# Optimization experiments

Measured on AMD Instinct MI355X. Metric: run time of the kernel, lower is better.

Reference implementation:

```python
import jax, jax.numpy as jnp
import numpy as np

B, N, IN_DIM, OUT_DIM, H = 8, 1024, 256, 256, 8
D = OUT_DIM // H  # support_dim = 32


def setup_inputs() -> dict:
    key = jax.random.key(0)
    k_a, k_x, k_w, k_f1, k_f2 = jax.random.split(key, 5)
    A = (jax.random.uniform(k_a, (B, N, N)) < 0.05).astype(jnp.float32)
    eye = jnp.eye(N, dtype=jnp.float32)
    A = jnp.maximum(A, eye[None, :, :])
    X = jax.random.normal(k_x, (B, N, IN_DIM), dtype=jnp.float32)
    std_w = 1.0 / np.sqrt(OUT_DIM)
    std_f = 1.0 / np.sqrt(D)
    weight = jax.random.uniform(k_w, (IN_DIM, OUT_DIM), minval=-std_w, maxval=std_w)
    fc1 = jax.random.uniform(k_f1, (H, D), minval=-std_f, maxval=std_f)
    fc2 = jax.random.uniform(k_f2, (H, D), minval=-std_f, maxval=std_f)
    return {"A": A, "X": X, "weight": weight, "fc1": fc1, "fc2": fc2}


def reference(A, X, weight, fc1, fc2):
    # inputs: [B, N, H, D]
    inputs = jnp.einsum('bni,io->bno', X, weight).reshape(B, N, H, D)
    # additive attention scores (rank-1 broadcast)
    self_s = jnp.einsum('bnhd,hd->bhn', inputs, fc1)   # [B,H,N] (query/self term)
    neigh_s = jnp.einsum('bnhd,hd->bhn', inputs, fc2)  # [B,H,N] (key/neighbor term)
    scores = jax.nn.leaky_relu(self_s[:, :, :, None] + neigh_s[:, :, None, :])  # [B,H,N,N]
    mask = (-1e9 * (1.0 - A))[:, None, :, :]  # [B,1,N,N]
    alphas = jax.nn.softmax(scores + mask, axis=-1)  # [B,H,N,N]
    out = jnp.einsum('bhnm,bmhd->bnhd', alphas, inputs).reshape(B, N, OUT_DIM)
    return jax.nn.relu(out)
```

## Files before the change

### kernel.cpp

```cpp
#include <hip/hip_runtime.h>

typedef unsigned short u16;
typedef __attribute__((ext_vector_type(8))) short short8;
typedef __attribute__((ext_vector_type(4))) float floatx4;

#define NB 8
#define NN 1024
#define KDIM 256
#define ODIM 256
#define NH 8
#define LDA 264
#define ECAP 256
#define ESTR 260

__device__ __forceinline__ u16 bf_rne(float x) {
    union { float f; unsigned u; } c{x};
    unsigned r = c.u + 0x7fff + ((c.u >> 16) & 1);
    return (u16)(r >> 16);
}
__device__ __forceinline__ float bf_f(u16 b) {
    union { unsigned u; float f; } c{(unsigned)b << 16};
    return c.f;
}

__global__ __launch_bounds__(256) void wprep(const float* __restrict__ W,
                                             u16* __restrict__ WhiT,
                                             u16* __restrict__ WloT) {
    __shared__ float tile[64][65];
    int bt = blockIdx.x;
    int kt = bt >> 2, ot = bt & 3;
    int tid = threadIdx.x;
    int r = tid >> 6, c = tid & 63;
#pragma unroll
    for (int rr = r; rr < 64; rr += 4)
        tile[rr][c] = W[(kt * 64 + rr) * ODIM + ot * 64 + c];
    __syncthreads();
#pragma unroll
    for (int oo = r; oo < 64; oo += 4) {
        float w = tile[c][oo];
        u16 h = bf_rne(w);
        u16 l = bf_rne(w - bf_f(h));
        WhiT[(ot * 64 + oo) * KDIM + kt * 64 + c] = h;
        WloT[(ot * 64 + oo) * KDIM + kt * 64 + c] = l;
    }
}

__global__ __launch_bounds__(256) void gemm_scores(
        const float* __restrict__ X, const u16* __restrict__ WhiT,
        const u16* __restrict__ WloT, const float* __restrict__ fc1,
        const float* __restrict__ fc2, float* __restrict__ inp,
        float* __restrict__ self_s, float* __restrict__ neigh_s) {
    __shared__ u16 ah_lds[16 * LDA];
    __shared__ u16 al_lds[16 * LDA];

    int tid = threadIdx.x;
    int w = tid >> 6, lane = tid & 63;
    int m = lane & 15, q = lane >> 4;
    int row0 = blockIdx.x * 16;

    const float4* Xr = (const float4*)(X + (size_t)row0 * KDIM);
#pragma unroll
    for (int p = 0; p < 4; ++p) {
        int f = p * 256 + tid;
        int r = f >> 6, c4 = (f & 63) * 4;
        float4 v = Xr[f];
        ushort4 hi, lo; u16 hh, ll;
#define SPLIT1(val, A, B) hh = bf_rne(val); ll = bf_rne((val) - bf_f(hh)); A = hh; B = ll;
        SPLIT1(v.x, hi.x, lo.x)
        SPLIT1(v.y, hi.y, lo.y)
        SPLIT1(v.z, hi.z, lo.z)
        SPLIT1(v.w, hi.w, lo.w)
        *(ushort4*)&ah_lds[r * LDA + c4] = hi;
        *(ushort4*)&al_lds[r * LDA + c4] = lo;
    }
    __syncthreads();

    floatx4 acc[4] = {{0,0,0,0},{0,0,0,0},{0,0,0,0},{0,0,0,0}};
#pragma unroll
    for (int k0 = 0; k0 < KDIM; k0 += 32) {
        short8 Ah = *(const short8*)&ah_lds[m * LDA + k0 + q * 8];
        short8 Al = *(const short8*)&al_lds[m * LDA + k0 + q * 8];
#pragma unroll
        for (int t = 0; t < 4; ++t) {
            int o = w * 64 + t * 16 + m;
            short8 Bh = *(const short8*)(WhiT + (size_t)o * KDIM + k0 + q * 8);
            short8 Bl = *(const short8*)(WloT + (size_t)o * KDIM + k0 + q * 8);
            acc[t] = __builtin_amdgcn_mfma_f32_16x16x32_bf16(Ah, Bh, acc[t], 0, 0, 0);
            acc[t] = __builtin_amdgcn_mfma_f32_16x16x32_bf16(Ah, Bl, acc[t], 0, 0, 0);
            acc[t] = __builtin_amdgcn_mfma_f32_16x16x32_bf16(Al, Bh, acc[t], 0, 0, 0);
        }
    }

#pragma unroll
    for (int t = 0; t < 4; ++t) {
        int col = w * 64 + t * 16 + m;
#pragma unroll
        for (int r = 0; r < 4; ++r)
            inp[(size_t)(row0 + q * 4 + r) * ODIM + col] = acc[t][r];
    }

    float f1[4], f2[4];
#pragma unroll
    for (int t = 0; t < 4; ++t) {
        int col = w * 64 + t * 16 + m;
        f1[t] = fc1[col];
        f2[t] = fc2[col];
    }
#pragma unroll
    for (int r = 0; r < 4; ++r) {
        float a0 = acc[0][r] * f1[0] + acc[1][r] * f1[1];
        float b0 = acc[0][r] * f2[0] + acc[1][r] * f2[1];
        float a1 = acc[2][r] * f1[2] + acc[3][r] * f1[3];
        float b1 = acc[2][r] * f2[2] + acc[3][r] * f2[3];
#pragma unroll
        for (int ofs = 8; ofs >= 1; ofs >>= 1) {
            a0 += __shfl_xor(a0, ofs);
            b0 += __shfl_xor(b0, ofs);
            a1 += __shfl_xor(a1, ofs);
            b1 += __shfl_xor(b1, ofs);
        }
        if (m == 0) {
            int n = row0 + q * 4 + r;
            int b = n >> 10, nn = n & 1023;
            self_s [((size_t)(b * NH + 2 * w) << 10) + nn] = a0;
            neigh_s[((size_t)(b * NH + 2 * w) << 10) + nn] = b0;
            self_s [((size_t)(b * NH + 2 * w + 1) << 10) + nn] = a1;
            neigh_s[((size_t)(b * NH + 2 * w + 1) << 10) + nn] = b1;
        }
    }
}

__global__ __launch_bounds__(256) void gat_agg(
        const float* __restrict__ A, const float* __restrict__ inp,
        const float* __restrict__ self_s, const float* __restrict__ neigh_s,
        float* __restrict__ out) {
    __shared__ u16 lst[NN];
    __shared__ float esc[NH][ESTR];
    __shared__ float red[4][256];
    __shared__ float hinv[NH];
    __shared__ int cnt;

    int bx = blockIdx.x;
    int b = bx & 7;
    int n = bx >> 3;
    int bn = (b << 10) | n;
    int tid = threadIdx.x;

    if (tid == 0) cnt = 0;
    __syncthreads();
    {
        float4 a4 = ((const float4*)(A + (size_t)bn * NN))[tid];
        int base = tid * 4;
        if (a4.x != 0.f) lst[atomicAdd(&cnt, 1)] = (u16)base;
        if (a4.y != 0.f) lst[atomicAdd(&cnt, 1)] = (u16)(base + 1);
        if (a4.z != 0.f) lst[atomicAdd(&cnt, 1)] = (u16)(base + 2);
        if (a4.w != 0.f) lst[atomicAdd(&cnt, 1)] = (u16)(base + 3);
    }
    __syncthreads();
    int nnz = cnt;
    if (nnz > ECAP) nnz = ECAP;

    int h = tid >> 5, j = tid & 31;
    const float* nsh = neigh_s + ((size_t)(b * NH + h) << 10);
    float selfv = self_s[((size_t)(b * NH + h) << 10) + n];
    float lsum = 0.f;
    for (int i = j; i < nnz; i += 32) {
        float s = selfv + nsh[lst[i]];
        s = s > 0.f ? s : 0.01f * s;
        float e = __expf(s);
        esc[h][i] = e;
        lsum += e;
    }
#pragma unroll
    for (int ofs = 16; ofs >= 1; ofs >>= 1)
        lsum += __shfl_xor(lsum, ofs);
    if (j == 0) hinv[h] = 1.f / lsum;
    __syncthreads();

    int wv = tid >> 6, lane = tid & 63;
    int hh = lane >> 3;
    const float4* ib = (const float4*)(inp + ((size_t)b << 10) * ODIM) + lane;
    floatx4 acc = {0.f, 0.f, 0.f, 0.f};
#pragma unroll 2
    for (int i = wv; i < nnz; i += 4) {
        float e = esc[hh][i];
        float4 v = ib[(size_t)lst[i] * 64];
        acc[0] = fmaf(e, v.x, acc[0]);
        acc[1] = fmaf(e, v.y, acc[1]);
        acc[2] = fmaf(e, v.z, acc[2]);
        acc[3] = fmaf(e, v.w, acc[3]);
    }
    *(floatx4*)&red[wv][lane * 4] = acc;
    __syncthreads();

    float r0 = red[0][tid] + red[1][tid] + red[2][tid] + red[3][tid];
    r0 *= hinv[tid >> 5];
    out[(size_t)bn * ODIM + tid] = r0 > 0.f ? r0 : 0.f;
}

extern "C" void kernel_launch(void* const* d_in, const int* in_sizes, int n_in,
                              void* d_out, int out_size, void* d_ws, size_t ws_size,
                              hipStream_t stream) {
    const float* A   = (const float*)d_in[0];
    const float* X   = (const float*)d_in[1];
    const float* W   = (const float*)d_in[2];
    const float* fc1 = (const float*)d_in[3];
    const float* fc2 = (const float*)d_in[4];
    float* out = (float*)d_out;

    char* ws = (char*)d_ws;
    const size_t MB = 1024u * 1024u;
    float* inp     = (float*)ws;
    u16*   WhiT    = (u16*)(ws + 8 * MB);
    u16*   WloT    = (u16*)(ws + 8 * MB + 128 * 1024);
    float* self_s  = (float*)(ws + 8 * MB + 256 * 1024);
    float* neigh_s = (float*)(ws + 8 * MB + 512 * 1024);

    wprep<<<16, 256, 0, stream>>>(W, WhiT, WloT);
    gemm_scores<<<NB * NN / 16, 256, 0, stream>>>(
        X, WhiT, WloT, fc1, fc2, inp, self_s, neigh_s);
    gat_agg<<<NB * NN, 256, 0, stream>>>(A, inp, self_s, neigh_s, out);
}
```

Baseline: 131.7 us.

## Fuse weight prep, GEMM and aggregation into one cooperative persistent kernel

Replaces the three launches with a single cooperative kernel of 1024 blocks that uses grid-wide syncs between weight splitting, the split-bf16 GEMM with score reduction, and the attention aggregation. Each block now covers half the output columns of a 16-row tile in the GEMM, then processes 8 destination rows in a loop for aggregation. The aim is to remove launch gaps and inter-kernel tails. In exchange it adds grid-sync cost and runs the aggregation with fewer, persistent blocks, which may hide memory latency less well. The old three-kernel path is kept as a fallback if the cooperative launch fails.

```diff
diff --git a/kernel.cpp b/kernel.cpp
--- a/kernel.cpp
+++ b/kernel.cpp
@@ -1,4 +1,7 @@
 #include <hip/hip_runtime.h>
+#include <hip/hip_cooperative_groups.h>
+
+namespace cg = cooperative_groups;
 
 typedef unsigned short u16;
 typedef __attribute__((ext_vector_type(8))) short short8;
@@ -22,6 +25,182 @@
     union { unsigned u; float f; } c{(unsigned)b << 16};
     return c.f;
 }
+#define SPLIT1(val, A_, B_) { u16 hh_ = bf_rne(val); u16 ll_ = bf_rne((val) - bf_f(hh_)); A_ = hh_; B_ = ll_; }
+
+__global__ __launch_bounds__(256, 4) void gat_fused(
+        const float* __restrict__ A, const float* __restrict__ X,
+        const float* __restrict__ W, const float* __restrict__ fc1,
+        const float* __restrict__ fc2, float* __restrict__ inp,
+        u16* __restrict__ WhiT, u16* __restrict__ WloT,
+        float* __restrict__ self_s, float* __restrict__ neigh_s,
+        float* __restrict__ out) {
+    __shared__ __align__(16) char smem[17408];
+    u16* ah_lds = (u16*)smem;
+    u16* al_lds = ah_lds + 16 * LDA;
+
+    int tid = threadIdx.x;
+    int bid = blockIdx.x;
+    int w = tid >> 6, lane = tid & 63;
+    int m = lane & 15, q = lane >> 4;
+
+    cg::grid_group grid = cg::this_grid();
+
+    if (bid < 16) {
+        float (*wtile)[65] = (float(*)[65])smem;
+        int kt = bid >> 2, ot = bid & 3;
+        int r = tid >> 6, c = tid & 63;
+#pragma unroll
+        for (int rr = r; rr < 64; rr += 4)
+            wtile[rr][c] = W[(kt * 64 + rr) * ODIM + ot * 64 + c];
+        __syncthreads();
+#pragma unroll
+        for (int oo = r; oo < 64; oo += 4) {
+            float wv = wtile[c][oo];
+            u16 h, l;
+            SPLIT1(wv, h, l)
+            WhiT[(ot * 64 + oo) * KDIM + kt * 64 + c] = h;
+            WloT[(ot * 64 + oo) * KDIM + kt * 64 + c] = l;
+        }
+        __syncthreads();
+    }
+
+    int rb = bid >> 1;
+    int row0 = rb * 16;
+    int cbase = (bid & 1) * 128;
+    {
+        const float4* Xr = (const float4*)(X + (size_t)row0 * KDIM);
+#pragma unroll
+        for (int p = 0; p < 4; ++p) {
+            int f = p * 256 + tid;
+            int r = f >> 6, c4 = (f & 63) * 4;
+            float4 v = Xr[f];
+            ushort4 hi, lo;
+            SPLIT1(v.x, hi.x, lo.x)
+            SPLIT1(v.y, hi.y, lo.y)
+            SPLIT1(v.z, hi.z, lo.z)
+            SPLIT1(v.w, hi.w, lo.w)
+            *(ushort4*)&ah_lds[r * LDA + c4] = hi;
+            *(ushort4*)&al_lds[r * LDA + c4] = lo;
+        }
+    }
+    if (bid < 16) __threadfence();
+    grid.sync();
+
+    floatx4 acc[2] = {{0, 0, 0, 0}, {0, 0, 0, 0}};
+#pragma unroll
+    for (int k0 = 0; k0 < KDIM; k0 += 32) {
+        short8 Ah = *(const short8*)&ah_lds[m * LDA + k0 + q * 8];
+        short8 Al = *(const short8*)&al_lds[m * LDA + k0 + q * 8];
+#pragma unroll
+        for (int t = 0; t < 2; ++t) {
+            int o = cbase + w * 32 + t * 16 + m;
+            short8 Bh = *(const short8*)(WhiT + (size_t)o * KDIM + k0 + q * 8);
+            short8 Bl = *(const short8*)(WloT + (size_t)o * KDIM + k0 + q * 8);
+            acc[t] = __builtin_amdgcn_mfma_f32_16x16x32_bf16(Ah, Bh, acc[t], 0, 0, 0);
+            acc[t] = __builtin_amdgcn_mfma_f32_16x16x32_bf16(Ah, Bl, acc[t], 0, 0, 0);
+            acc[t] = __builtin_amdgcn_mfma_f32_16x16x32_bf16(Al, Bh, acc[t], 0, 0, 0);
+        }
+    }
+#pragma unroll
+    for (int t = 0; t < 2; ++t) {
+        int col = cbase + w * 32 + t * 16 + m;
+#pragma unroll
+        for (int r = 0; r < 4; ++r)
+            inp[(size_t)(row0 + q * 4 + r) * ODIM + col] = acc[t][r];
+    }
+    {
+        int hd = (bid & 1) * 4 + w;
+        float f1[2], f2[2];
+#pragma unroll
+        for (int t = 0; t < 2; ++t) {
+            int col = hd * 32 + t * 16 + m;
+            f1[t] = fc1[col];
+            f2[t] = fc2[col];
+        }
+#pragma unroll
+        for (int r = 0; r < 4; ++r) {
+            float a = acc[0][r] * f1[0] + acc[1][r] * f1[1];
+            float bb = acc[0][r] * f2[0] + acc[1][r] * f2[1];
+#pragma unroll
+            for (int ofs = 8; ofs >= 1; ofs >>= 1) {
+                a += __shfl_xor(a, ofs);
+                bb += __shfl_xor(bb, ofs);
+            }
+            if (m == 0) {
+                int n = row0 + q * 4 + r;
+                int b = n >> 10, nn = n & 1023;
+                self_s [((size_t)(b * NH + hd) << 10) + nn] = a;
+                neigh_s[((size_t)(b * NH + hd) << 10) + nn] = bb;
+            }
+        }
+    }
+    __threadfence();
+    grid.sync();
+
+    u16*  lst  = (u16*)smem;
+    float* esc = (float*)(smem + 2048);
+    float* red = (float*)(smem + 10368);
+    float* hinv = (float*)(smem + 14464);
+    int*  cntp = (int*)(smem + 14496);
+
+    int b2 = bid >> 7;
+    int h = tid >> 5, j = tid & 31;
+    int hh = lane >> 3;
+    const float4* ib = (const float4*)(inp + ((size_t)b2 << 10) * ODIM) + lane;
+
+    for (int rr = 0; rr < 8; ++rr) {
+        int bn = bid * 8 + rr;
+        int n = bn & 1023;
+
+        if (tid == 0) *cntp = 0;
+        __syncthreads();
+        {
+            float4 a4 = ((const float4*)(A + (size_t)bn * NN))[tid];
+            int base = tid * 4;
+            if (a4.x != 0.f) lst[atomicAdd(cntp, 1)] = (u16)base;
+            if (a4.y != 0.f) lst[atomicAdd(cntp, 1)] = (u16)(base + 1);
+            if (a4.z != 0.f) lst[atomicAdd(cntp, 1)] = (u16)(base + 2);
+            if (a4.w != 0.f) lst[atomicAdd(cntp, 1)] = (u16)(base + 3);
+        }
+        __syncthreads();
+        int nnz = *cntp;
+        if (nnz > ECAP) nnz = ECAP;
+
+        const float* nsh = neigh_s + ((size_t)(b2 * NH + h) << 10);
+        float selfv = self_s[((size_t)(b2 * NH + h) << 10) + n];
+        float lsum = 0.f;
+        for (int i = j; i < nnz; i += 32) {
+            float s = selfv + nsh[lst[i]];
+            s = s > 0.f ? s : 0.01f * s;
+            float e = __expf(s);
+            esc[h * ESTR + i] = e;
+            lsum += e;
+        }
+#pragma unroll
+        for (int ofs = 16; ofs >= 1; ofs >>= 1)
+            lsum += __shfl_xor(lsum, ofs);
+        if (j == 0) hinv[h] = 1.f / lsum;
+        __syncthreads();
+
+        floatx4 acc2 = {0.f, 0.f, 0.f, 0.f};
+#pragma unroll 4
+        for (int i = w; i < nnz; i += 4) {
+            float e = esc[hh * ESTR + i];
+            float4 v = ib[(size_t)lst[i] * 64];
+            acc2[0] = fmaf(e, v.x, acc2[0]);
+            acc2[1] = fmaf(e, v.y, acc2[1]);
+            acc2[2] = fmaf(e, v.z, acc2[2]);
+            acc2[3] = fmaf(e, v.w, acc2[3]);
+        }
+        *(floatx4*)&red[w * 256 + lane * 4] = acc2;
+        __syncthreads();
+
+        float r0 = red[tid] + red[256 + tid] + red[512 + tid] + red[768 + tid];
+        r0 *= hinv[tid >> 5];
+        out[(size_t)bn * ODIM + tid] = r0 > 0.f ? r0 : 0.f;
+        __syncthreads();
+    }
+}
 
 __global__ __launch_bounds__(256) void wprep(const float* __restrict__ W,
                                              u16* __restrict__ WhiT,
@@ -38,8 +217,8 @@
 #pragma unroll
     for (int oo = r; oo < 64; oo += 4) {
         float w = tile[c][oo];
-        u16 h = bf_rne(w);
-        u16 l = bf_rne(w - bf_f(h));
+        u16 h, l;
+        SPLIT1(w, h, l)
         WhiT[(ot * 64 + oo) * KDIM + kt * 64 + c] = h;
         WloT[(ot * 64 + oo) * KDIM + kt * 64 + c] = l;
     }
@@ -64,8 +243,7 @@
         int f = p * 256 + tid;
         int r = f >> 6, c4 = (f & 63) * 4;
         float4 v = Xr[f];
-        ushort4 hi, lo; u16 hh, ll;
-#define SPLIT1(val, A, B) hh = bf_rne(val); ll = bf_rne((val) - bf_f(hh)); A = hh; B = ll;
+        ushort4 hi, lo;
         SPLIT1(v.x, hi.x, lo.x)
         SPLIT1(v.y, hi.y, lo.y)
         SPLIT1(v.z, hi.z, lo.z)
@@ -216,8 +394,16 @@
     float* self_s  = (float*)(ws + 8 * MB + 256 * 1024);
     float* neigh_s = (float*)(ws + 8 * MB + 512 * 1024);
 
-    wprep<<<16, 256, 0, stream>>>(W, WhiT, WloT);
-    gemm_scores<<<NB * NN / 16, 256, 0, stream>>>(
-        X, WhiT, WloT, fc1, fc2, inp, self_s, neigh_s);
-    gat_agg<<<NB * NN, 256, 0, stream>>>(A, inp, self_s, neigh_s, out);
-}
+    void* args[] = {(void*)&A, (void*)&X, (void*)&W, (void*)&fc1, (void*)&fc2,
+                    (void*)&inp, (void*)&WhiT, (void*)&WloT, (void*)&self_s,
+                    (void*)&neigh_s, (void*)&out};
+    hipError_t e = hipLaunchCooperativeKernel((const void*)gat_fused,
+                                              dim3(1024), dim3(256),
+                                              args, 0, stream);
+    if (e != hipSuccess) {
+        wprep<<<16, 256, 0, stream>>>(W, WhiT, WloT);
+        gemm_scores<<<NB * NN / 16, 256, 0, stream>>>(
+            X, WhiT, WloT, fc1, fc2, inp, self_s, neigh_s);
+        gat_agg<<<NB * NN, 256, 0, stream>>>(A, inp, self_s, neigh_s, out);
+    }
+}
```

After: 476.4 us. +261.9%, slower.
